# Optimization experiments

Measured on AMD Instinct MI355X. Metric: run time of the kernel, lower is better.

Reference implementation:

```python
import jax, jax.numpy as jnp
import numpy as np

N = 8192
E = 262144

def gcn_conv(x, W, b, row, col, w):
    # PyG GCNConv with self-loops already appended to (row, col, w).
    h = x @ W                                   # [N, out]
    deg = jax.ops.segment_sum(w, col, num_segments=N)
    dinv = jnp.where(deg > 0, jax.lax.rsqrt(deg), 0.0)
    norm = dinv[row] * w * dinv[col]            # [E+N]
    out = jax.ops.segment_sum(norm[:, None] * h[row], col, num_segments=N)
    return out + b

def setup_inputs() -> dict:
    key = jax.random.key(0)
    ks = jax.random.split(key, 10)
    return {
        "x": jax.random.normal(ks[0], (N, 512), jnp.float32),
        "edge_index": jax.random.randint(ks[1], (2, E), 0, N, jnp.int64),
        "edge_weight": jax.random.uniform(ks[2], (E,), jnp.float32),
        "noise": jax.random.normal(ks[3], (N, 64), jnp.float32),
        "W1": jax.random.normal(ks[4], (512, 256), jnp.float32) * 0.05,
        "b1": jnp.zeros((256,), jnp.float32),
        "W2": jax.random.normal(ks[5], (256, 256), jnp.float32) * 0.05,
        "b2": jnp.zeros((256,), jnp.float32),
        "Wm": jax.random.normal(ks[6], (256, 64), jnp.float32) * 0.05,
        "bm": jnp.zeros((64,), jnp.float32),
        "Ws": jax.random.normal(ks[7], (256, 64), jnp.float32) * 0.05,
        "bs": jnp.zeros((64,), jnp.float32),
    }

def reference(x, edge_index, edge_weight, noise, W1, b1, W2, b2, Wm, bm, Ws, bs):
    # add self-loops once (weight 1.0), shared by all GCN layers
    loop = jnp.arange(N, dtype=edge_index.dtype)
    row = jnp.concatenate([edge_index[0], loop])
    col = jnp.concatenate([edge_index[1], loop])
    w = jnp.concatenate([edge_weight, jnp.ones((N,), edge_weight.dtype)])

    h = jax.nn.relu(gcn_conv(x, W1, b1, row, col, w))
    h = jax.nn.relu(gcn_conv(h, W2, b2, row, col, w))
    mean = jax.nn.relu(gcn_conv(h, Wm, bm, row, col, w))
    log_std = jax.nn.relu(gcn_conv(h, Ws, bs, row, col, w))
    z = noise * jnp.exp(log_std) + mean          # [N, 64]
    adj = jax.nn.sigmoid(z @ z.T)                # [N, N]
    return jnp.triu(adj, k=1)
```

## Files before the change

### kernel.cpp

```cpp
#include <hip/hip_runtime.h>
#include <hip/hip_bf16.h>

#define NN 8192
#define NE 262144

typedef __attribute__((ext_vector_type(8))) short bf16x8;
typedef __attribute__((ext_vector_type(4))) float f32x4;

__global__ __launch_bounds__(256) void k_init(float* __restrict__ deg, int* __restrict__ counts,
                                              int* __restrict__ cnt2) {
  int i = blockIdx.x * 256 + threadIdx.x;
  if (i < NN) { deg[i] = 1.0f; counts[i] = 0; cnt2[i] = 0; }
}

__global__ __launch_bounds__(256) void k_count(const int* __restrict__ ei, const float* __restrict__ w,
                                               float* __restrict__ deg, int* __restrict__ counts) {
  int e = blockIdx.x * 256 + threadIdx.x;
  if (e < NE) {
    int c = ei[NE + e];
    atomicAdd(&deg[c], w[e]);
    atomicAdd(&counts[c], 1);
  }
}

__global__ __launch_bounds__(256) void k_dinv(const float* __restrict__ deg, float* __restrict__ dinv) {
  int i = blockIdx.x * 256 + threadIdx.x;
  if (i < NN) dinv[i] = rsqrtf(deg[i]);
}

__global__ __launch_bounds__(1024) void k_scan(const int* __restrict__ counts, int* __restrict__ offs) {
  __shared__ int part[1024];
  int t = threadIdx.x;
  int base = t * 8;
  int local[8];
  int s = 0;
#pragma unroll
  for (int j = 0; j < 8; ++j) { local[j] = counts[base + j]; s += local[j]; }
  part[t] = s;
  __syncthreads();
  for (int off = 1; off < 1024; off <<= 1) {
    int v = (t >= off) ? part[t - off] : 0;
    __syncthreads();
    part[t] += v;
    __syncthreads();
  }
  int run = (t > 0) ? part[t - 1] : 0;
#pragma unroll
  for (int j = 0; j < 8; ++j) { offs[base + j] = run; run += local[j]; }
  if (t == 1023) offs[NN] = run;
}

__global__ __launch_bounds__(256) void k_scatter(const int* __restrict__ ei, const float* __restrict__ w,
                                                 const float* __restrict__ dinv, const int* __restrict__ offs,
                                                 int* __restrict__ cnt2, int* __restrict__ csr_row,
                                                 float* __restrict__ csr_val) {
  int e = blockIdx.x * 256 + threadIdx.x;
  if (e < NE) {
    int r = ei[e], c = ei[NE + e];
    int slot = offs[c] + atomicAdd(&cnt2[c], 1);
    csr_row[slot] = r;
    csr_val[slot] = dinv[r] * w[e] * dinv[c];
  }
}

__global__ __launch_bounds__(256) void k_gemm(const float* __restrict__ A, const float* __restrict__ B,
                                              float* __restrict__ C, int M, int K, int Nc) {
  __shared__ float As[16][68];
  __shared__ float Bs[16][64];
  int t = threadIdx.x;
  int tx = t & 15, ty = t >> 4;
  int m0 = blockIdx.y * 64, n0 = blockIdx.x * 64;
  int la_r = t >> 2;
  int la_c = (t & 3) * 4;
  int lb_r = t >> 4;
  int lb_c = (t & 15) * 4;
  const float* Aptr = A + (size_t)(m0 + la_r) * K + la_c;
  const float* Bptr = B + (size_t)lb_r * Nc + n0 + lb_c;
  float acc[4][4] = {};
  for (int k0 = 0; k0 < K; k0 += 16) {
    float4 av = *(const float4*)(Aptr + k0);
    float4 bv = *(const float4*)(Bptr + (size_t)k0 * Nc);
    __syncthreads();
    As[la_c + 0][la_r] = av.x;
    As[la_c + 1][la_r] = av.y;
    As[la_c + 2][la_r] = av.z;
    As[la_c + 3][la_r] = av.w;
    *(float4*)&Bs[lb_r][lb_c] = bv;
    __syncthreads();
#pragma unroll
    for (int kk = 0; kk < 16; ++kk) {
      f32x4 a4 = *(const f32x4*)&As[kk][ty * 4];
      f32x4 b4 = *(const f32x4*)&Bs[kk][tx * 4];
#pragma unroll
      for (int i = 0; i < 4; ++i)
#pragma unroll
        for (int j = 0; j < 4; ++j)
          acc[i][j] = fmaf(a4[i], b4[j], acc[i][j]);
    }
  }
#pragma unroll
  for (int i = 0; i < 4; ++i) {
    f32x4 v = {acc[i][0], acc[i][1], acc[i][2], acc[i][3]};
    *(f32x4*)&C[(size_t)(m0 + ty * 4 + i) * Nc + n0 + tx * 4] = v;
  }
}

__global__ void k_agg(const float* __restrict__ t, const float* __restrict__ dinv,
                      const int* __restrict__ csr_row, const float* __restrict__ csr_val,
                      const int* __restrict__ offs, const float* __restrict__ bias,
                      float* __restrict__ outb, int D) {
  int c = blockIdx.x;
  int d = threadIdx.x;
  float di = dinv[c];
  float acc = di * di * t[(size_t)c * D + d];
  int s0 = offs[c], s1 = offs[c + 1];
  for (int s = s0; s < s1; ++s) {
    acc += csr_val[s] * t[(size_t)csr_row[s] * D + d];
  }
  outb[(size_t)c * D + d] = fmaxf(acc + bias[d], 0.0f);
}

__global__ __launch_bounds__(256) void k_cat(const float* __restrict__ Wm, const float* __restrict__ Wsw,
                                             const float* __restrict__ bm, const float* __restrict__ bsv,
                                             float* __restrict__ Wcat, float* __restrict__ bcat) {
  int idx = blockIdx.x * 256 + threadIdx.x;
  if (idx < 256 * 128) {
    int k = idx >> 7, c = idx & 127;
    Wcat[idx] = (c < 64) ? Wm[k * 64 + c] : Wsw[k * 64 + (c - 64)];
  } else if (idx < 256 * 128 + 128) {
    int c = idx - 256 * 128;
    bcat[c] = (c < 64) ? bm[c] : bsv[c - 64];
  }
}

__global__ __launch_bounds__(256) void k_z(const float* __restrict__ gms, const float* __restrict__ noise,
                                           __hip_bfloat16* __restrict__ zh, __hip_bfloat16* __restrict__ zl) {
  int idx = blockIdx.x * 256 + threadIdx.x;
  int i = idx >> 6, k = idx & 63;
  float mean = gms[(size_t)i * 128 + k];
  float ls = gms[(size_t)i * 128 + 64 + k];
  float z = noise[idx] * __expf(ls) + mean;
  __hip_bfloat16 h = __float2bfloat16(z);
  zh[idx] = h;
  zl[idx] = __float2bfloat16(z - __bfloat162float(h));
}

__global__ __launch_bounds__(256) void k_final(const short* __restrict__ zh, const short* __restrict__ zl,
                                               float* __restrict__ out) {
  int ti = blockIdx.y, tj = blockIdx.x;
  int ri0 = ti * 128, cj0 = tj * 128;
  if (tj < ti) {
    f32x4 zz = {};
    int tr = threadIdx.x >> 5;
    int tc = (threadIdx.x & 31) << 2;
    float* base = out + (size_t)(ri0 + tr) * NN + cj0 + tc;
#pragma unroll
    for (int rr = 0; rr < 128; rr += 8)
      *(f32x4*)(base + (size_t)rr * NN) = zz;
    return;
  }
  int wv = threadIdx.x >> 6;
  int lane = threadIdx.x & 63;
  int wr = wv >> 1, wc = wv & 1;
  int lr = lane & 15;
  int lk = (lane >> 4) << 3;
  int arow = ri0 + wr * 64 + lr;
  int brow = cj0 + wc * 64 + lr;

  bf16x8 ah[4][2], al[4][2];
#pragma unroll
  for (int rb = 0; rb < 4; ++rb)
#pragma unroll
    for (int ks = 0; ks < 2; ++ks) {
      int o = (arow + rb * 16) * 64 + ks * 32 + lk;
      ah[rb][ks] = *(const bf16x8*)(zh + o);
      al[rb][ks] = *(const bf16x8*)(zl + o);
    }
  f32x4 acc[4][4] = {};
#pragma unroll
  for (int cb = 0; cb < 4; ++cb) {
    bf16x8 bh[2], bl[2];
#pragma unroll
    for (int ks = 0; ks < 2; ++ks) {
      int o = (brow + cb * 16) * 64 + ks * 32 + lk;
      bh[ks] = *(const bf16x8*)(zh + o);
      bl[ks] = *(const bf16x8*)(zl + o);
    }
#pragma unroll
    for (int rb = 0; rb < 4; ++rb) {
      f32x4 c = acc[rb][cb];
#pragma unroll
      for (int ks = 0; ks < 2; ++ks) {
        c = __builtin_amdgcn_mfma_f32_16x16x32_bf16(ah[rb][ks], bh[ks], c, 0, 0, 0);
        c = __builtin_amdgcn_mfma_f32_16x16x32_bf16(ah[rb][ks], bl[ks], c, 0, 0, 0);
        c = __builtin_amdgcn_mfma_f32_16x16x32_bf16(al[rb][ks], bh[ks], c, 0, 0, 0);
      }
      acc[rb][cb] = c;
    }
  }
  int orow = ri0 + wr * 64 + ((lane >> 4) << 2);
  int ocol = cj0 + wc * 64 + (lane & 15);
#pragma unroll
  for (int rb = 0; rb < 4; ++rb)
#pragma unroll
    for (int cb = 0; cb < 4; ++cb)
#pragma unroll
      for (int r = 0; r < 4; ++r) {
        int row = orow + rb * 16 + r;
        int col = ocol + cb * 16;
        float v = acc[rb][cb][r];
        float sg = 1.0f / (1.0f + __expf(-v));
        out[(size_t)row * NN + col] = (col > row) ? sg : 0.0f;
      }
}

extern "C" void kernel_launch(void* const* d_in, const int* in_sizes, int n_in,
                              void* d_out, int out_size, void* d_ws, size_t ws_size,
                              hipStream_t stream) {
  (void)in_sizes; (void)n_in; (void)out_size; (void)ws_size;
  const float* x     = (const float*)d_in[0];
  const int*   ei    = (const int*)d_in[1];
  const float* ew    = (const float*)d_in[2];
  const float* noise = (const float*)d_in[3];
  const float* W1    = (const float*)d_in[4];
  const float* b1    = (const float*)d_in[5];
  const float* W2    = (const float*)d_in[6];
  const float* b2    = (const float*)d_in[7];
  const float* Wm    = (const float*)d_in[8];
  const float* bm    = (const float*)d_in[9];
  const float* Wsw   = (const float*)d_in[10];
  const float* bsv   = (const float*)d_in[11];
  float* out = (float*)d_out;

  char* wsb = (char*)d_ws;
  size_t off = 0;
  auto bump = [&](size_t bytes) -> void* {
    void* p = wsb + off;
    off += (bytes + 255) & ~(size_t)255;
    return p;
  };
  float* deg     = (float*)bump((size_t)NN * 4);
  float* dinv    = (float*)bump((size_t)NN * 4);
  int*   counts  = (int*)bump((size_t)NN * 4);
  int*   offs    = (int*)bump((size_t)(NN + 1) * 4);
  int*   cnt2    = (int*)bump((size_t)NN * 4);
  int*   csr_row = (int*)bump((size_t)NE * 4);
  float* csr_val = (float*)bump((size_t)NE * 4);
  float* bufA    = (float*)bump((size_t)NN * 256 * 4);
  float* bufB    = (float*)bump((size_t)NN * 256 * 4);
  float* bufC    = (float*)bump((size_t)NN * 128 * 4);
  float* bufG    = (float*)bump((size_t)NN * 128 * 4);
  float* Wcat    = (float*)bump((size_t)256 * 128 * 4);
  float* bcat    = (float*)bump((size_t)128 * 4);
  __hip_bfloat16* zh = (__hip_bfloat16*)bump((size_t)NN * 64 * 2);
  __hip_bfloat16* zl = (__hip_bfloat16*)bump((size_t)NN * 64 * 2);

  k_init<<<NN / 256, 256, 0, stream>>>(deg, counts, cnt2);
  k_count<<<NE / 256, 256, 0, stream>>>(ei, ew, deg, counts);
  k_dinv<<<NN / 256, 256, 0, stream>>>(deg, dinv);
  k_scan<<<1, 1024, 0, stream>>>(counts, offs);
  k_scatter<<<NE / 256, 256, 0, stream>>>(ei, ew, dinv, offs, cnt2, csr_row, csr_val);

  k_gemm<<<dim3(4, 128), 256, 0, stream>>>(x, W1, bufA, NN, 512, 256);
  k_agg<<<NN, 256, 0, stream>>>(bufA, dinv, csr_row, csr_val, offs, b1, bufB, 256);
  k_gemm<<<dim3(4, 128), 256, 0, stream>>>(bufB, W2, bufA, NN, 256, 256);
  k_agg<<<NN, 256, 0, stream>>>(bufA, dinv, csr_row, csr_val, offs, b2, bufB, 256);
  k_cat<<<129, 256, 0, stream>>>(Wm, Wsw, bm, bsv, Wcat, bcat);
  k_gemm<<<dim3(2, 128), 256, 0, stream>>>(bufB, Wcat, bufC, NN, 256, 128);
  k_agg<<<NN, 128, 0, stream>>>(bufC, dinv, csr_row, csr_val, offs, bcat, bufG, 128);
  k_z<<<NN * 64 / 256, 256, 0, stream>>>(bufG, noise, zh, zl);
  k_final<<<dim3(64, 64), 256, 0, stream>>>((const short*)zh, (const short*)zl, out);
}
```

Baseline: 341.0 us.

## Split edge aggregation across four wavefronts with vectorized row loads and smem reduce

The aggregation kernel now stages each node's CSR indices and weights in shared memory, splits the edge list across four 64-lane wavefronts that each read float4/float2 row slices, and reduces the partial sums through shared memory. The intent is more parallelism per destination node and fewer serial dependent loads per thread than one-thread-per-feature serial loops. It also removes the separate dinv kernel, recomputing rsqrt of degree inline in scatter and aggregation. The costs are an extra shared-memory reduction and barriers per block.

```diff
diff --git a/kernel.cpp b/kernel.cpp
--- a/kernel.cpp
+++ b/kernel.cpp
@@ -23,11 +23,6 @@
   }
 }
 
-__global__ __launch_bounds__(256) void k_dinv(const float* __restrict__ deg, float* __restrict__ dinv) {
-  int i = blockIdx.x * 256 + threadIdx.x;
-  if (i < NN) dinv[i] = rsqrtf(deg[i]);
-}
-
 __global__ __launch_bounds__(1024) void k_scan(const int* __restrict__ counts, int* __restrict__ offs) {
   __shared__ int part[1024];
   int t = threadIdx.x;
@@ -51,7 +46,7 @@
 }
 
 __global__ __launch_bounds__(256) void k_scatter(const int* __restrict__ ei, const float* __restrict__ w,
-                                                 const float* __restrict__ dinv, const int* __restrict__ offs,
+                                                 const float* __restrict__ deg, const int* __restrict__ offs,
                                                  int* __restrict__ cnt2, int* __restrict__ csr_row,
                                                  float* __restrict__ csr_val) {
   int e = blockIdx.x * 256 + threadIdx.x;
@@ -59,7 +54,7 @@
     int r = ei[e], c = ei[NE + e];
     int slot = offs[c] + atomicAdd(&cnt2[c], 1);
     csr_row[slot] = r;
-    csr_val[slot] = dinv[r] * w[e] * dinv[c];
+    csr_val[slot] = rsqrtf(deg[r]) * w[e] * rsqrtf(deg[c]);
   }
 }
 
@@ -105,19 +100,59 @@
   }
 }
 
-__global__ void k_agg(const float* __restrict__ t, const float* __restrict__ dinv,
-                      const int* __restrict__ csr_row, const float* __restrict__ csr_val,
-                      const int* __restrict__ offs, const float* __restrict__ bias,
-                      float* __restrict__ outb, int D) {
+template <int D>
+__global__ __launch_bounds__(256) void k_agg(const float* __restrict__ t, const float* __restrict__ deg,
+                                             const int* __restrict__ csr_row, const float* __restrict__ csr_val,
+                                             const int* __restrict__ offs, const float* __restrict__ bias,
+                                             float* __restrict__ outb) {
+  constexpr int V = D / 64;
+  __shared__ int   srow[256];
+  __shared__ float sval[256];
+  __shared__ float sacc[4][D];
   int c = blockIdx.x;
-  int d = threadIdx.x;
-  float di = dinv[c];
-  float acc = di * di * t[(size_t)c * D + d];
+  int tid = threadIdx.x;
+  int w = tid >> 6, lane = tid & 63;
+  int d0 = lane * V;
+  float acc[V];
+#pragma unroll
+  for (int j = 0; j < V; ++j) acc[j] = 0.0f;
   int s0 = offs[c], s1 = offs[c + 1];
-  for (int s = s0; s < s1; ++s) {
-    acc += csr_val[s] * t[(size_t)csr_row[s] * D + d];
-  }
-  outb[(size_t)c * D + d] = fmaxf(acc + bias[d], 0.0f);
+  for (int base = s0; base < s1; base += 256) {
+    int cnt = s1 - base; if (cnt > 256) cnt = 256;
+    __syncthreads();
+    if (tid < cnt) { srow[tid] = csr_row[base + tid]; sval[tid] = csr_val[base + tid]; }
+    __syncthreads();
+    for (int s = w; s < cnt; s += 4) {
+      int r = srow[s];
+      float v = sval[s];
+      const float* p = t + (size_t)r * D + d0;
+      if constexpr (V == 4) {
+        float4 pv = *(const float4*)p;
+        acc[0] = fmaf(v, pv.x, acc[0]);
+        acc[1] = fmaf(v, pv.y, acc[1]);
+        acc[2] = fmaf(v, pv.z, acc[2]);
+        acc[3] = fmaf(v, pv.w, acc[3]);
+      } else {
+        float2 pv = *(const float2*)p;
+        acc[0] = fmaf(v, pv.x, acc[0]);
+        acc[1] = fmaf(v, pv.y, acc[1]);
+      }
+    }
+  }
+#pragma unroll
+  for (int j = 0; j < V; ++j) sacc[w][d0 + j] = acc[j];
+  __syncthreads();
+  if (tid < 64) {
+    float di = rsqrtf(deg[c]);
+    float selfw = di * di;
+#pragma unroll
+    for (int j = 0; j < V; ++j) {
+      int d = tid * V + j;
+      float a = sacc[0][d] + sacc[1][d] + sacc[2][d] + sacc[3][d];
+      a = fmaf(selfw, t[(size_t)c * D + d], a);
+      outb[(size_t)c * D + d] = fmaxf(a + bias[d], 0.0f);
+    }
+  }
 }
 
 __global__ __launch_bounds__(256) void k_cat(const float* __restrict__ Wm, const float* __restrict__ Wsw,
@@ -240,7 +275,6 @@
     return p;
   };
   float* deg     = (float*)bump((size_t)NN * 4);
-  float* dinv    = (float*)bump((size_t)NN * 4);
   int*   counts  = (int*)bump((size_t)NN * 4);
   int*   offs    = (int*)bump((size_t)(NN + 1) * 4);
   int*   cnt2    = (int*)bump((size_t)NN * 4);
@@ -257,17 +291,16 @@
 
   k_init<<<NN / 256, 256, 0, stream>>>(deg, counts, cnt2);
   k_count<<<NE / 256, 256, 0, stream>>>(ei, ew, deg, counts);
-  k_dinv<<<NN / 256, 256, 0, stream>>>(deg, dinv);
   k_scan<<<1, 1024, 0, stream>>>(counts, offs);
-  k_scatter<<<NE / 256, 256, 0, stream>>>(ei, ew, dinv, offs, cnt2, csr_row, csr_val);
+  k_scatter<<<NE / 256, 256, 0, stream>>>(ei, ew, deg, offs, cnt2, csr_row, csr_val);
 
   k_gemm<<<dim3(4, 128), 256, 0, stream>>>(x, W1, bufA, NN, 512, 256);
-  k_agg<<<NN, 256, 0, stream>>>(bufA, dinv, csr_row, csr_val, offs, b1, bufB, 256);
+  k_agg<256><<<NN, 256, 0, stream>>>(bufA, deg, csr_row, csr_val, offs, b1, bufB);
   k_gemm<<<dim3(4, 128), 256, 0, stream>>>(bufB, W2, bufA, NN, 256, 256);
-  k_agg<<<NN, 256, 0, stream>>>(bufA, dinv, csr_row, csr_val, offs, b2, bufB, 256);
+  k_agg<256><<<NN, 256, 0, stream>>>(bufA, deg, csr_row, csr_val, offs, b2, bufB);
   k_cat<<<129, 256, 0, stream>>>(Wm, Wsw, bm, bsv, Wcat, bcat);
   k_gemm<<<dim3(2, 128), 256, 0, stream>>>(bufB, Wcat, bufC, NN, 256, 128);
-  k_agg<<<NN, 128, 0, stream>>>(bufC, dinv, csr_row, csr_val, offs, bcat, bufG, 128);
+  k_agg<128><<<NN, 256, 0, stream>>>(bufC, deg, csr_row, csr_val, offs, bcat, bufG);
   k_z<<<NN * 64 / 256, 256, 0, stream>>>(bufG, noise, zh, zl);
   k_final<<<dim3(64, 64), 256, 0, stream>>>((const short*)zh, (const short*)zl, out);
 }
```

After: 274.0 us. 19.6% less time.
